# Optimization experiments

Hardware: AMD Instinct MI355X
Metric: run time of the kernel (lower is better)

Reference implementation:

```python
import jax, jax.numpy as jnp
import numpy as np

D_MODEL = 1024
NUM_HEADS = 16
HEAD_DIM = D_MODEL // NUM_HEADS


def setup_inputs() -> dict:
    key = jax.random.key(0)
    ks = jax.random.split(key, 12)
    B, S = 2, 2048
    scale = 1.0 / np.sqrt(D_MODEL)
    inp = {
        "x": jax.random.normal(ks[0], (B, S, D_MODEL), dtype=jnp.float32),
        "docking_scores": jax.random.uniform(ks[1], (B, S), dtype=jnp.float32),
        "q_w": jax.random.normal(ks[2], (D_MODEL, D_MODEL), dtype=jnp.float32) * scale,
        "q_b": jnp.zeros((D_MODEL,), dtype=jnp.float32),
        "k_w": jax.random.normal(ks[3], (D_MODEL, D_MODEL), dtype=jnp.float32) * scale,
        "k_b": jnp.zeros((D_MODEL,), dtype=jnp.float32),
        "v_w": jax.random.normal(ks[4], (D_MODEL, D_MODEL), dtype=jnp.float32) * scale,
        "v_b": jnp.zeros((D_MODEL,), dtype=jnp.float32),
        "o_w": jax.random.normal(ks[5], (D_MODEL, D_MODEL), dtype=jnp.float32) * scale,
        "o_b": jnp.zeros((D_MODEL,), dtype=jnp.float32),
        "alpha": jnp.float32(0.5),
    }
    return inp


def reference(x, docking_scores, q_w, q_b, k_w, k_b, v_w, v_b, o_w, o_b, alpha):
    B, S, _ = x.shape
    # Projections; weights stored as (in, out) so y = x @ W + b
    def proj(w, b):
        y = jnp.einsum('bsd,de->bse', x, w) + b
        return y.reshape(B, S, NUM_HEADS, HEAD_DIM).transpose(0, 2, 1, 3)  # (B,H,S,hd)
    Q = proj(q_w, q_b)
    K = proj(k_w, k_b)
    V = proj(v_w, v_b)
    scores = jnp.einsum('bhqd,bhkd->bhqk', Q, K) / np.sqrt(HEAD_DIM)
    attn = jax.nn.softmax(scores, axis=-1)  # (B,H,S,S)
    # post-softmax docking blend, broadcast over heads and query positions
    ds = docking_scores[:, None, None, :]  # (B,1,1,S)
    attn = (1.0 - alpha) * attn + alpha * ds
    ctx = jnp.einsum('bhqk,bhkd->bhqd', attn, V)
    ctx = ctx.transpose(0, 2, 1, 3).reshape(B, S, D_MODEL)
    return jnp.einsum('bsd,de->bse', ctx, o_w) + o_b
```

## Files before the change

kernel.cpp:

```cpp
#include <hip/hip_runtime.h>
#include <hip/hip_bf16.h>

typedef __attribute__((ext_vector_type(8)))  short bf16x8;
typedef __attribute__((ext_vector_type(4)))  float f32x4;
typedef __attribute__((ext_vector_type(16))) float f32x16;
typedef __attribute__((ext_vector_type(4)))  int   i32x4;
typedef __attribute__((ext_vector_type(4)))  unsigned short u16x4;
typedef __attribute__((ext_vector_type(8)))  unsigned short u16x8;

__device__ __forceinline__ unsigned short f2bf(float f) {
    unsigned int u = __builtin_bit_cast(unsigned int, f);
    u += 0x7FFFu + ((u >> 16) & 1u);
    return (unsigned short)(u >> 16);
}
__device__ __forceinline__ float bf2f(unsigned short h) {
    unsigned int u = ((unsigned int)h) << 16;
    return __builtin_bit_cast(float, u);
}
__device__ __forceinline__ bf16x8 ld16(const unsigned short* p) {
    return *reinterpret_cast<const bf16x8*>(p);
}
__device__ __forceinline__ float fexp2(float x) {
    float r; asm("v_exp_f32 %0, %1" : "=v"(r) : "v"(x)); return r;
}
__device__ __forceinline__ float frcp(float x) {
    float r; asm("v_rcp_f32 %0, %1" : "=v"(r) : "v"(x)); return r;
}
__device__ __forceinline__ void pswap(unsigned int& a, unsigned int& b) {
    asm("v_permlane32_swap_b32 %0, %1" : "+v"(a), "+v"(b));
}

__global__ void prep_kernel(const float* __restrict__ x,
                            const float* __restrict__ q_w, const float* __restrict__ k_w,
                            const float* __restrict__ v_w, const float* __restrict__ o_w,
                            unsigned short* __restrict__ WT, unsigned short* __restrict__ xb) {
    __shared__ float tile[32][33];
    const int tx = threadIdx.x, ty = threadIdx.y;
    if (blockIdx.z < 4) {
        const float* W = (blockIdx.z == 0) ? q_w : (blockIdx.z == 1) ? k_w : (blockIdx.z == 2) ? v_w : o_w;
        unsigned short* dst = WT + (size_t)blockIdx.z * 1024 * 1024;
        int n0 = blockIdx.x * 32, k0 = blockIdx.y * 32;
#pragma unroll
        for (int j = 0; j < 4; ++j)
            tile[ty + j*8][tx] = W[(size_t)(k0 + ty + j*8) * 1024 + n0 + tx];
        __syncthreads();
#pragma unroll
        for (int j = 0; j < 4; ++j)
            dst[(size_t)(n0 + ty + j*8) * 1024 + k0 + tx] = f2bf(tile[tx][ty + j*8]);
    } else {
        const int t = ty * 32 + tx;
        const int bid = blockIdx.y * 32 + blockIdx.x;
#pragma unroll
        for (int c = 0; c < 2; ++c) {
            const int i = bid * 512 + c * 256 + t;
            f32x4 a = reinterpret_cast<const f32x4*>(x)[i*2];
            f32x4 b = reinterpret_cast<const f32x4*>(x)[i*2+1];
            u16x8 o;
            o[0]=f2bf(a[0]); o[1]=f2bf(a[1]); o[2]=f2bf(a[2]); o[3]=f2bf(a[3]);
            o[4]=f2bf(b[0]); o[5]=f2bf(b[1]); o[6]=f2bf(b[2]); o[7]=f2bf(b[3]);
            reinterpret_cast<u16x8*>(xb)[i] = o;
        }
    }
}


__global__ __launch_bounds__(256) void gemm_qkv(
    const unsigned short* __restrict__ A,
    const unsigned short* __restrict__ WT,
    const float* __restrict__ qb, const float* __restrict__ kbias, const float* __restrict__ vbias,
    unsigned short* __restrict__ Qo, unsigned short* __restrict__ KFo, unsigned short* __restrict__ VFo)
{
    __shared__ __align__(16) unsigned short As[2][128*64];
    __shared__ __align__(16) unsigned short Bs[2][128*64];
    const int tid = threadIdx.x, lane = tid & 63, w = tid >> 6;
    const int wm = w >> 1, wn = w & 1;
    const int m0 = blockIdx.y * 128, n0 = blockIdx.x * 128;
    const int K = 1024;
    const int sr = tid >> 3, ssl = tid & 7;
    const int ssw = (ssl ^ (sr & 7)) << 3;
    f32x4 acc[4][4] = {};

    auto stage = [&](int buf, int k0) {
#pragma unroll
        for (int j = 0; j < 4; ++j) {
            const int c = j*256 + tid, r = j*32 + sr;
            __builtin_amdgcn_global_load_lds(
                (const __attribute__((address_space(1))) void*)&A[(size_t)(m0+r)*K + k0 + ssw],
                (__attribute__((address_space(3))) void*)&As[buf][(size_t)c*8], 16, 0, 0);
            __builtin_amdgcn_global_load_lds(
                (const __attribute__((address_space(1))) void*)&WT[(size_t)(n0+r)*K + k0 + ssw],
                (__attribute__((address_space(3))) void*)&Bs[buf][(size_t)c*8], 16, 0, 0);
        }
    };

    stage(0, 0);
#pragma unroll 1
    for (int t = 0; t < 16; ++t) {
        __syncthreads();
        if (t < 15) stage((t + 1) & 1, (t + 1) * 64);
        const unsigned short* pa = &As[t & 1][0];
        const unsigned short* pb = &Bs[t & 1][0];
#pragma unroll
        for (int kc = 0; kc < 2; ++kc) {
            bf16x8 af[4], bfr[4];
            const int slog = kc*4 + (lane >> 4);
#pragma unroll
            for (int t2 = 0; t2 < 4; ++t2) {
                const int row = wm*64 + t2*16 + (lane & 15);
                af[t2]  = ld16(&pa[row*64 + ((slog ^ (row & 7)) << 3)]);
                const int col = wn*64 + t2*16 + (lane & 15);
                bfr[t2] = ld16(&pb[col*64 + ((slog ^ (col & 7)) << 3)]);
            }
#pragma unroll
            for (int mt = 0; mt < 4; ++mt)
#pragma unroll
                for (int nt = 0; nt < 4; ++nt)
                    acc[mt][nt] = __builtin_amdgcn_mfma_f32_16x16x32_bf16(af[mt], bfr[nt], acc[mt][nt], 0, 0, 0);
        }
    }
    const int mat = n0 >> 10;
    if (mat == 2) {
#pragma unroll
        for (int mt = 0; mt < 4; ++mt)
#pragma unroll
        for (int nt = 0; nt < 4; ++nt) {
            const int nl = (n0 & 1023) + wn*64 + nt*16 + (lane & 15);
            const int h = nl >> 6, hd = nl & 63;
            const int mbase = m0 + wm*64 + mt*16 + ((lane >> 4) << 2);
            const int b = mbase >> 11, s = mbase & 2047;
            const float bv = vbias[nl];
            u16x4 pk;
#pragma unroll
            for (int r = 0; r < 4; ++r) pk[r] = f2bf(acc[mt][nt][r] + bv);
            const size_t off = (size_t)((b << 4) | h) * 131072 + (s >> 6) * 4096 + (hd >> 5) * 2048
                             + ((s >> 4) & 3) * 512 + ((s >> 3) & 1) * 256 + (hd & 31) * 8 + (s & 7);
            *reinterpret_cast<u16x4*>(&VFo[off]) = pk;
        }
    } else if (mat == 1) {
#pragma unroll
        for (int mt = 0; mt < 4; ++mt)
#pragma unroll
        for (int nt = 0; nt < 4; ++nt) {
            const int nl = (n0 & 1023) + wn*64 + nt*16 + (lane & 15);
            const int h = nl >> 6, hd = nl & 63;
            const int mbase = m0 + wm*64 + mt*16 + ((lane >> 4) << 2);
            const float bv = kbias[nl];
#pragma unroll
            for (int r = 0; r < 4; ++r) {
                const int mm2 = mbase + r, b = mm2 >> 11, s = mm2 & 2047;
                const size_t off = (size_t)((b << 4) | h) * 131072 + (s >> 5) * 2048 + (hd >> 4) * 512
                                 + ((hd >> 3) & 1) * 256 + (s & 31) * 8 + (hd & 7);
                KFo[off] = f2bf(acc[mt][nt][r] + bv);
            }
        }
    } else {
        const float scale = 0.180336881f;
#pragma unroll
        for (int mt = 0; mt < 4; ++mt)
#pragma unroll
        for (int nt = 0; nt < 4; ++nt) {
            const int nl = (n0 & 1023) + wn*64 + nt*16 + (lane & 15);
            const int h = nl >> 6, hd = nl & 63;
            const int mbase = m0 + wm*64 + mt*16 + ((lane >> 4) << 2);
            const float bv = qb[nl];
#pragma unroll
            for (int r = 0; r < 4; ++r) {
                const int mm2 = mbase + r, b = mm2 >> 11, s = mm2 & 2047;
                Qo[((size_t)((b << 4) | h) * 2048 + s) * 64 + hd] = f2bf((acc[mt][nt][r] + bv) * scale);
            }
        }
    }
}

__global__ __launch_bounds__(256) void gemm_o(
    const unsigned short* __restrict__ A, const unsigned short* __restrict__ WT,
    const float* __restrict__ bias, float* __restrict__ Cout)
{
    __shared__ __align__(16) unsigned short As[2][128*64];
    __shared__ __align__(16) unsigned short Bs[2][128*64];
    const int tid = threadIdx.x, lane = tid & 63, w = tid >> 6;
    const int wm = w >> 1, wn = w & 1;
    const int m0 = blockIdx.y * 128, n0 = blockIdx.x * 128;
    const int K = 1024;
    const int sr = tid >> 3, ssl = tid & 7;
    const int ssw = (ssl ^ (sr & 7)) << 3;
    f32x4 acc[4][4] = {};

    auto stage = [&](int buf, int k0) {
#pragma unroll
        for (int j = 0; j < 4; ++j) {
            const int c = j*256 + tid, r = j*32 + sr;
            __builtin_amdgcn_global_load_lds(
                (const __attribute__((address_space(1))) void*)&A[(size_t)(m0+r)*K + k0 + ssw],
                (__attribute__((address_space(3))) void*)&As[buf][(size_t)c*8], 16, 0, 0);
            __builtin_amdgcn_global_load_lds(
                (const __attribute__((address_space(1))) void*)&WT[(size_t)(n0+r)*K + k0 + ssw],
                (__attribute__((address_space(3))) void*)&Bs[buf][(size_t)c*8], 16, 0, 0);
        }
    };

    stage(0, 0);
#pragma unroll 1
    for (int t = 0; t < 16; ++t) {
        __syncthreads();
        if (t < 15) stage((t + 1) & 1, (t + 1) * 64);
        const unsigned short* pa = &As[t & 1][0];
        const unsigned short* pb = &Bs[t & 1][0];
#pragma unroll
        for (int kc = 0; kc < 2; ++kc) {
            bf16x8 af[4], bfr[4];
            const int slog = kc*4 + (lane >> 4);
#pragma unroll
            for (int t2 = 0; t2 < 4; ++t2) {
                const int row = wm*64 + t2*16 + (lane & 15);
                af[t2]  = ld16(&pa[row*64 + ((slog ^ (row & 7)) << 3)]);
                const int col = wn*64 + t2*16 + (lane & 15);
                bfr[t2] = ld16(&pb[col*64 + ((slog ^ (col & 7)) << 3)]);
            }
#pragma unroll
            for (int mt = 0; mt < 4; ++mt)
#pragma unroll
                for (int nt = 0; nt < 4; ++nt)
                    acc[mt][nt] = __builtin_amdgcn_mfma_f32_16x16x32_bf16(af[mt], bfr[nt], acc[mt][nt], 0, 0, 0);
        }
    }
#pragma unroll
    for (int mt = 0; mt < 4; ++mt)
#pragma unroll
    for (int nt = 0; nt < 4; ++nt) {
        const int n = n0 + wn*64 + nt*16 + (lane & 15);
        const int mbase = m0 + wm*64 + mt*16 + ((lane >> 4) << 2);
        const float bv = bias[n];
#pragma unroll
        for (int r = 0; r < 4; ++r)
            Cout[(size_t)(mbase + r) * 1024 + n] = acc[mt][nt][r] + bv;
    }
}

__global__ void dock_c_kernel(const float* __restrict__ ds, const unsigned short* __restrict__ VF,
                              float* __restrict__ cvec) {
    __shared__ float red[256];
    const int bh = blockIdx.x;
    const int b = bh >> 4;
    const int t = threadIdx.x;
    const int lane = t & 63, t2 = (t >> 6) & 1, k4 = t >> 7;
    const int hi = lane >> 5;
    const unsigned short* VFb = VF + (size_t)bh * 131072;
    const float* dsb = ds + b * 2048;
    float sum = 0.f;
    for (int kvt = k4; kvt < 32; kvt += 2) {
#pragma unroll
        for (int ks = 0; ks < 4; ++ks) {
            bf16x8 v = ld16(VFb + kvt*4096 + t2*2048 + ks*512 + lane*8);
            const int kv0 = kvt*64 + ks*16 + hi*8;
            f32x4 d0 = *reinterpret_cast<const f32x4*>(&dsb[kv0]);
            f32x4 d1 = *reinterpret_cast<const f32x4*>(&dsb[kv0 + 4]);
            sum += d0[0]*bf2f((unsigned short)v[0]) + d0[1]*bf2f((unsigned short)v[1])
                 + d0[2]*bf2f((unsigned short)v[2]) + d0[3]*bf2f((unsigned short)v[3])
                 + d1[0]*bf2f((unsigned short)v[4]) + d1[1]*bf2f((unsigned short)v[5])
                 + d1[2]*bf2f((unsigned short)v[6]) + d1[3]*bf2f((unsigned short)v[7]);
        }
    }
    red[t] = sum;
    __syncthreads();
    if (t < 64) {
        const int ln = t & 31, tt2 = t >> 5;
        const int base = tt2 * 64 + ln;
        cvec[bh * 64 + tt2 * 32 + ln] = red[base] + red[base + 32] + red[base + 128] + red[base + 160];
    }
}

__global__ __launch_bounds__(256, 2) void attn_kernel(
    const unsigned short* __restrict__ Qp,
    const unsigned short* __restrict__ KF,
    const unsigned short* __restrict__ VF,
    const float* __restrict__ cvec,
    const float* __restrict__ alpha_p,
    unsigned short* __restrict__ ctx)
{
    __shared__ __align__(16) unsigned short Ks[2][4096];
    __shared__ __align__(16) unsigned short Vs[2][4096];
    const int tid = threadIdx.x, lane = tid & 63, w = tid >> 6;
    const int hi = lane >> 5, ln = lane & 31;
    const int wg = blockIdx.x;
    const int swz = (wg & 7) * 64 + (wg >> 3);
    const int bh = swz >> 4, qt = swz & 15;
    const int q0 = qt * 128 + w * 32;
    const size_t hb = (size_t)bh * (2048 * 64);
    const float alpha = *alpha_p;

    const unsigned short* KFb = KF + (size_t)bh * 131072;
    const unsigned short* VFb = VF + (size_t)bh * 131072;
    const int fo = lane * 8;

    bf16x8 qf[4];
    {
        const unsigned short* qr = &Qp[hb + (size_t)(q0 + ln) * 64 + hi * 8];
#pragma unroll
        for (int ks = 0; ks < 4; ++ks) qf[ks] = ld16(qr + ks * 16);
    }

    const short one_bf = (short)0x3F80;
    const bf16x8 onesf = {one_bf, one_bf, one_bf, one_bf, one_bf, one_bf, one_bf, one_bf};

    f32x16 oacc0 = {}, oacc1 = {}, lacc = {};

    auto stage = [&](int buf, int it) {
#pragma unroll
        for (int p = 0; p < 2; ++p) {
            __builtin_amdgcn_global_load_lds(
                (const __attribute__((address_space(1))) void*)(KFb + it*4096 + p*2048 + tid*8),
                (__attribute__((address_space(3))) void*)&Ks[buf][p*2048 + tid*8], 16, 0, 0);
            __builtin_amdgcn_global_load_lds(
                (const __attribute__((address_space(1))) void*)(VFb + it*4096 + p*2048 + tid*8),
                (__attribute__((address_space(3))) void*)&Vs[buf][p*2048 + tid*8], 16, 0, 0);
        }
    };

    bf16x8 kf[8];
    auto ldk = [&](const unsigned short* base) {
#pragma unroll
        for (int t2 = 0; t2 < 2; ++t2)
#pragma unroll
        for (int ks = 0; ks < 4; ++ks)
            kf[t2*4+ks] = ld16(base + t2*2048 + ks*512 + fo);
    };

    stage(0, 0);
    __syncthreads();
    stage(1, 1);
    ldk(&Ks[0][0]);
    f32x16 sA0 = {}, sA1 = {}, sB0 = {}, sB1 = {};
#pragma unroll
    for (int ks = 0; ks < 4; ++ks) {
        sA0 = __builtin_amdgcn_mfma_f32_32x32x16_bf16(kf[ks],   qf[ks], sA0, 0, 0, 0);
        sA1 = __builtin_amdgcn_mfma_f32_32x32x16_bf16(kf[4+ks], qf[ks], sA1, 0, 0, 0);
    }

    auto step = [&](f32x16& sc0, f32x16& sc1, f32x16& sn0, f32x16& sn1, int buf, int it) {
        bf16x8 vf[8];
#pragma unroll
        for (int t2 = 0; t2 < 2; ++t2)
#pragma unroll
        for (int ks = 0; ks < 4; ++ks)
            vf[t2*4+ks] = ld16(&Vs[buf][t2*2048 + ks*512 + fo]);
        __syncthreads();
        if (it + 2 < 32) stage(buf, it + 2);
        const bool more = (it + 1 < 32);
        if (more) ldk(&Ks[buf ^ 1][0]);
        __builtin_amdgcn_s_setprio(1);
        if (more) {
            sn0 = {}; sn1 = {};
#pragma unroll
            for (int ks = 0; ks < 4; ++ks) {
                sn0 = __builtin_amdgcn_mfma_f32_32x32x16_bf16(kf[ks],   qf[ks], sn0, 0, 0, 0);
                sn1 = __builtin_amdgcn_mfma_f32_32x32x16_bf16(kf[4+ks], qf[ks], sn1, 0, 0, 0);
            }
        }
        float p0a[16], p1a[16];
#pragma unroll
        for (int r = 0; r < 16; ++r) {
            p0a[r] = fexp2(sc0[r]);
            p1a[r] = fexp2(sc1[r]);
        }
        unsigned int Wp0[4][2], Wp1[4][2];
#pragma unroll
        for (int m4 = 0; m4 < 4; ++m4)
#pragma unroll
        for (int jj = 0; jj < 2; ++jj) {
            asm("v_cvt_pk_bf16_f32 %0, %1, %2" : "=v"(Wp0[m4][jj]) : "v"(p0a[m4*4+jj*2]), "v"(p0a[m4*4+jj*2+1]));
            asm("v_cvt_pk_bf16_f32 %0, %1, %2" : "=v"(Wp1[m4][jj]) : "v"(p1a[m4*4+jj*2]), "v"(p1a[m4*4+jj*2+1]));
        }
#pragma unroll
        for (int ks = 0; ks < 4; ++ks) {
            const int tp = ks & 1;
            unsigned int a0, a1, b0, b1;
            if (ks < 2) { a0 = Wp0[2*tp][0]; a1 = Wp0[2*tp][1]; b0 = Wp0[2*tp+1][0]; b1 = Wp0[2*tp+1][1]; }
            else        { a0 = Wp1[2*tp][0]; a1 = Wp1[2*tp][1]; b0 = Wp1[2*tp+1][0]; b1 = Wp1[2*tp+1][1]; }
            pswap(a0, b0);
            pswap(a1, b1);
            i32x4 pw;
            pw[0] = (int)a0; pw[1] = (int)a1; pw[2] = (int)b0; pw[3] = (int)b1;
            bf16x8 pf = __builtin_bit_cast(bf16x8, pw);
            oacc0 = __builtin_amdgcn_mfma_f32_32x32x16_bf16(pf, vf[ks],   oacc0, 0, 0, 0);
            oacc1 = __builtin_amdgcn_mfma_f32_32x32x16_bf16(pf, vf[4+ks], oacc1, 0, 0, 0);
            lacc  = __builtin_amdgcn_mfma_f32_32x32x16_bf16(pf, onesf,    lacc,  0, 0, 0);
        }
        __builtin_amdgcn_s_setprio(0);
    };

#pragma unroll 1
    for (int ii = 0; ii < 16; ++ii) {
        step(sA0, sA1, sB0, sB1, 0, ii*2);
        step(sB0, sB1, sA0, sA1, 1, ii*2 + 1);
    }

    const int b = bh >> 4, h = bh & 15;
    const float a1f = 1.f - alpha;
    const float cv0 = alpha * cvec[bh*64 + ln];
    const float cv1 = alpha * cvec[bh*64 + 32 + ln];
#pragma unroll
    for (int m4 = 0; m4 < 4; ++m4) {
#pragma unroll
        for (int r3 = 0; r3 < 4; ++r3) {
            const int row = m4*8 + hi*4 + r3;
            const int s = q0 + row;
            const float iv = frcp(lacc[m4*4 + r3]);
            unsigned short* orow = &ctx[((size_t)(b*2048 + s))*1024 + h*64 + ln];
            orow[0]  = f2bf(a1f * oacc0[m4*4+r3] * iv + cv0);
            orow[32] = f2bf(a1f * oacc1[m4*4+r3] * iv + cv1);
        }
    }
}

extern "C" void kernel_launch(void* const* d_in, const int* in_sizes, int n_in,
                              void* d_out, int out_size, void* d_ws, size_t ws_size,
                              hipStream_t stream) {
    const float* x     = (const float*)d_in[0];
    const float* ds    = (const float*)d_in[1];
    const float* q_w   = (const float*)d_in[2];
    const float* q_b   = (const float*)d_in[3];
    const float* k_w   = (const float*)d_in[4];
    const float* k_b   = (const float*)d_in[5];
    const float* v_w   = (const float*)d_in[6];
    const float* v_b   = (const float*)d_in[7];
    const float* o_w   = (const float*)d_in[8];
    const float* o_b   = (const float*)d_in[9];
    const float* alpha = (const float*)d_in[10];

    char* ws = (char*)d_ws;
    const size_t MB = 1024 * 1024;
    unsigned short* xb   = (unsigned short*)(ws);
    unsigned short* wT   = (unsigned short*)(ws + 8  * MB);
    unsigned short* Qb   = (unsigned short*)(ws + 16 * MB);
    unsigned short* KFb  = (unsigned short*)(ws + 24 * MB);
    unsigned short* VFb  = (unsigned short*)(ws + 32 * MB);
    float*          cvec = (float*)         (ws + 40 * MB);
    unsigned short* ctxb = xb;

    dim3 tb(32, 8);
    dim3 tg(32, 32, 5);
    prep_kernel<<<tg, tb, 0, stream>>>(x, q_w, k_w, v_w, o_w, wT, xb);

    dim3 gqkv(24, 32);
    gemm_qkv<<<gqkv, 256, 0, stream>>>(xb, wT, q_b, k_b, v_b, Qb, KFb, VFb);

    dock_c_kernel<<<32, 256, 0, stream>>>(ds, VFb, cvec);

    attn_kernel<<<512, 256, 0, stream>>>(Qb, KFb, VFb, cvec, alpha, ctxb);

    dim3 go(8, 32);
    gemm_o<<<go, 256, 0, stream>>>(ctxb, wT + (size_t)3 * MB, o_b, (float*)d_out);
}
```

Baseline: 126.3 us.

## Double KV tile size per stage to halve barriers in attention loop

The attention kernel now stages two 64-key K/V tiles per LDS buffer (8192 elements each), so each loop iteration processes 128 keys with one barrier and one async global-to-LDS stage instead of two. QK for the second half-tile overlaps softmax/PV of the first half, and QK for the next buffer overlaps the second half's PV. LDS use doubles to 64 KB per block, which may limit the two-blocks-per-CU occupancy target.

```diff
diff --git a/kernel.cpp b/kernel.cpp
--- a/kernel.cpp
+++ b/kernel.cpp
@@ -278,8 +278,8 @@
     const float* __restrict__ alpha_p,
     unsigned short* __restrict__ ctx)
 {
-    __shared__ __align__(16) unsigned short Ks[2][4096];
-    __shared__ __align__(16) unsigned short Vs[2][4096];
+    __shared__ __align__(16) unsigned short Ks[2][8192];
+    __shared__ __align__(16) unsigned short Vs[2][8192];
     const int tid = threadIdx.x, lane = tid & 63, w = tid >> 6;
     const int hi = lane >> 5, ln = lane & 31;
     const int wg = blockIdx.x;
@@ -305,58 +305,42 @@
 
     f32x16 oacc0 = {}, oacc1 = {}, lacc = {};
 
-    auto stage = [&](int buf, int it) {
-#pragma unroll
-        for (int p = 0; p < 2; ++p) {
-            __builtin_amdgcn_global_load_lds(
-                (const __attribute__((address_space(1))) void*)(KFb + it*4096 + p*2048 + tid*8),
+    auto stage2 = [&](int buf, int t2) {
+#pragma unroll
+        for (int p = 0; p < 4; ++p) {
+            __builtin_amdgcn_global_load_lds(
+                (const __attribute__((address_space(1))) void*)(KFb + t2*8192 + p*2048 + tid*8),
                 (__attribute__((address_space(3))) void*)&Ks[buf][p*2048 + tid*8], 16, 0, 0);
             __builtin_amdgcn_global_load_lds(
-                (const __attribute__((address_space(1))) void*)(VFb + it*4096 + p*2048 + tid*8),
+                (const __attribute__((address_space(1))) void*)(VFb + t2*8192 + p*2048 + tid*8),
                 (__attribute__((address_space(3))) void*)&Vs[buf][p*2048 + tid*8], 16, 0, 0);
         }
     };
 
     bf16x8 kf[8];
-    auto ldk = [&](const unsigned short* base) {
+    auto qk = [&](const unsigned short* base, f32x16& s0, f32x16& s1) {
 #pragma unroll
         for (int t2 = 0; t2 < 2; ++t2)
 #pragma unroll
         for (int ks = 0; ks < 4; ++ks)
             kf[t2*4+ks] = ld16(base + t2*2048 + ks*512 + fo);
-    };
-
-    stage(0, 0);
-    __syncthreads();
-    stage(1, 1);
-    ldk(&Ks[0][0]);
-    f32x16 sA0 = {}, sA1 = {}, sB0 = {}, sB1 = {};
-#pragma unroll
-    for (int ks = 0; ks < 4; ++ks) {
-        sA0 = __builtin_amdgcn_mfma_f32_32x32x16_bf16(kf[ks],   qf[ks], sA0, 0, 0, 0);
-        sA1 = __builtin_amdgcn_mfma_f32_32x32x16_bf16(kf[4+ks], qf[ks], sA1, 0, 0, 0);
-    }
-
-    auto step = [&](f32x16& sc0, f32x16& sc1, f32x16& sn0, f32x16& sn1, int buf, int it) {
-        bf16x8 vf[8];
+        s0 = {}; s1 = {};
+#pragma unroll
+        for (int ks = 0; ks < 4; ++ks) {
+            s0 = __builtin_amdgcn_mfma_f32_32x32x16_bf16(kf[ks],   qf[ks], s0, 0, 0, 0);
+            s1 = __builtin_amdgcn_mfma_f32_32x32x16_bf16(kf[4+ks], qf[ks], s1, 0, 0, 0);
+        }
+    };
+
+    auto ldv = [&](bf16x8 (&vf)[8], const unsigned short* base) {
 #pragma unroll
         for (int t2 = 0; t2 < 2; ++t2)
 #pragma unroll
         for (int ks = 0; ks < 4; ++ks)
-            vf[t2*4+ks] = ld16(&Vs[buf][t2*2048 + ks*512 + fo]);
-        __syncthreads();
-        if (it + 2 < 32) stage(buf, it + 2);
-        const bool more = (it + 1 < 32);
-        if (more) ldk(&Ks[buf ^ 1][0]);
-        __builtin_amdgcn_s_setprio(1);
-        if (more) {
-            sn0 = {}; sn1 = {};
-#pragma unroll
-            for (int ks = 0; ks < 4; ++ks) {
-                sn0 = __builtin_amdgcn_mfma_f32_32x32x16_bf16(kf[ks],   qf[ks], sn0, 0, 0, 0);
-                sn1 = __builtin_amdgcn_mfma_f32_32x32x16_bf16(kf[4+ks], qf[ks], sn1, 0, 0, 0);
-            }
-        }
+            vf[t2*4+ks] = ld16(base + t2*2048 + ks*512 + fo);
+    };
+
+    auto smpv = [&](f32x16& sc0, f32x16& sc1, bf16x8 (&vf)[8]) {
         float p0a[16], p1a[16];
 #pragma unroll
         for (int r = 0; r < 16; ++r) {
@@ -386,13 +370,30 @@
             oacc1 = __builtin_amdgcn_mfma_f32_32x32x16_bf16(pf, vf[4+ks], oacc1, 0, 0, 0);
             lacc  = __builtin_amdgcn_mfma_f32_32x32x16_bf16(pf, onesf,    lacc,  0, 0, 0);
         }
-        __builtin_amdgcn_s_setprio(0);
-    };
+    };
+
+    stage2(0, 0);
+    __syncthreads();
+    stage2(1, 1);
+    f32x16 sA0, sA1, sB0, sB1;
+    qk(&Ks[0][0], sA0, sA1);
 
 #pragma unroll 1
     for (int ii = 0; ii < 16; ++ii) {
-        step(sA0, sA1, sB0, sB1, 0, ii*2);
-        step(sB0, sB1, sA0, sA1, 1, ii*2 + 1);
+        const int b = ii & 1;
+        bf16x8 vf0[8], vf1[8];
+        ldv(vf0, &Vs[b][0]);
+        __builtin_amdgcn_s_setprio(1);
+        qk(&Ks[b][4096], sB0, sB1);
+        smpv(sA0, sA1, vf0);
+        __builtin_amdgcn_s_setprio(0);
+        ldv(vf1, &Vs[b][4096]);
+        __syncthreads();
+        if (ii + 2 < 16) stage2(b, ii + 2);
+        __builtin_amdgcn_s_setprio(1);
+        if (ii + 1 < 16) qk(&Ks[b ^ 1][0], sA0, sA1);
+        smpv(sB0, sB1, vf1);
+        __builtin_amdgcn_s_setprio(0);
     }
 
     const int b = bh >> 4, h = bh & 15;
```

Result: no change. 126.6 us (+0.3%).

## Fuse docking dot-product into QKV epilogue and replace ones-MFMA row sum

Applied to the files above, without the earlier changes.

Removes the separate dock_c_kernel by accumulating docking-weighted V sums with atomicAdd in the V-projection epilogue of gemm_qkv, after zeroing cvec with a memset. In attention, the softmax denominator is now computed by scalar adds of the exp values plus a lane swap and shared-memory broadcast, instead of an extra MFMA against a ones vector. This drops one kernel launch and a third of the PV MFMAs per step. In exchange it adds many global atomics (with nondeterministic summation order), a memset, and VALU adds in the inner loop.

```diff
diff --git a/kernel.cpp b/kernel.cpp
--- a/kernel.cpp
+++ b/kernel.cpp
@@ -68,7 +68,9 @@
     const unsigned short* __restrict__ A,
     const unsigned short* __restrict__ WT,
     const float* __restrict__ qb, const float* __restrict__ kbias, const float* __restrict__ vbias,
-    unsigned short* __restrict__ Qo, unsigned short* __restrict__ KFo, unsigned short* __restrict__ VFo)
+    const float* __restrict__ dsv,
+    unsigned short* __restrict__ Qo, unsigned short* __restrict__ KFo, unsigned short* __restrict__ VFo,
+    float* __restrict__ cvec)
 {
     __shared__ __align__(16) unsigned short As[2][128*64];
     __shared__ __align__(16) unsigned short Bs[2][128*64];
@@ -130,11 +132,15 @@
             const int b = mbase >> 11, s = mbase & 2047;
             const float bv = vbias[nl];
             u16x4 pk;
-#pragma unroll
-            for (int r = 0; r < 4; ++r) pk[r] = f2bf(acc[mt][nt][r] + bv);
+            float v0 = acc[mt][nt][0] + bv, v1 = acc[mt][nt][1] + bv;
+            float v2 = acc[mt][nt][2] + bv, v3 = acc[mt][nt][3] + bv;
+            pk[0] = f2bf(v0); pk[1] = f2bf(v1); pk[2] = f2bf(v2); pk[3] = f2bf(v3);
             const size_t off = (size_t)((b << 4) | h) * 131072 + (s >> 6) * 4096 + (hd >> 5) * 2048
                              + ((s >> 4) & 3) * 512 + ((s >> 3) & 1) * 256 + (hd & 31) * 8 + (s & 7);
             *reinterpret_cast<u16x4*>(&VFo[off]) = pk;
+            f32x4 d4 = *reinterpret_cast<const f32x4*>(&dsv[b * 2048 + s]);
+            float part = d4[0]*v0 + d4[1]*v1 + d4[2]*v2 + d4[3]*v3;
+            atomicAdd(&cvec[(size_t)((b << 4) | h) * 64 + hd], part);
         }
     } else if (mat == 1) {
 #pragma unroll
@@ -237,39 +243,6 @@
     }
 }
 
-__global__ void dock_c_kernel(const float* __restrict__ ds, const unsigned short* __restrict__ VF,
-                              float* __restrict__ cvec) {
-    __shared__ float red[256];
-    const int bh = blockIdx.x;
-    const int b = bh >> 4;
-    const int t = threadIdx.x;
-    const int lane = t & 63, t2 = (t >> 6) & 1, k4 = t >> 7;
-    const int hi = lane >> 5;
-    const unsigned short* VFb = VF + (size_t)bh * 131072;
-    const float* dsb = ds + b * 2048;
-    float sum = 0.f;
-    for (int kvt = k4; kvt < 32; kvt += 2) {
-#pragma unroll
-        for (int ks = 0; ks < 4; ++ks) {
-            bf16x8 v = ld16(VFb + kvt*4096 + t2*2048 + ks*512 + lane*8);
-            const int kv0 = kvt*64 + ks*16 + hi*8;
-            f32x4 d0 = *reinterpret_cast<const f32x4*>(&dsb[kv0]);
-            f32x4 d1 = *reinterpret_cast<const f32x4*>(&dsb[kv0 + 4]);
-            sum += d0[0]*bf2f((unsigned short)v[0]) + d0[1]*bf2f((unsigned short)v[1])
-                 + d0[2]*bf2f((unsigned short)v[2]) + d0[3]*bf2f((unsigned short)v[3])
-                 + d1[0]*bf2f((unsigned short)v[4]) + d1[1]*bf2f((unsigned short)v[5])
-                 + d1[2]*bf2f((unsigned short)v[6]) + d1[3]*bf2f((unsigned short)v[7]);
-        }
-    }
-    red[t] = sum;
-    __syncthreads();
-    if (t < 64) {
-        const int ln = t & 31, tt2 = t >> 5;
-        const int base = tt2 * 64 + ln;
-        cvec[bh * 64 + tt2 * 32 + ln] = red[base] + red[base + 32] + red[base + 128] + red[base + 160];
-    }
-}
-
 __global__ __launch_bounds__(256, 2) void attn_kernel(
     const unsigned short* __restrict__ Qp,
     const unsigned short* __restrict__ KF,
@@ -280,6 +253,7 @@
 {
     __shared__ __align__(16) unsigned short Ks[2][4096];
     __shared__ __align__(16) unsigned short Vs[2][4096];
+    __shared__ float sml[4][32];
     const int tid = threadIdx.x, lane = tid & 63, w = tid >> 6;
     const int hi = lane >> 5, ln = lane & 31;
     const int wg = blockIdx.x;
@@ -300,10 +274,8 @@
         for (int ks = 0; ks < 4; ++ks) qf[ks] = ld16(qr + ks * 16);
     }
 
-    const short one_bf = (short)0x3F80;
-    const bf16x8 onesf = {one_bf, one_bf, one_bf, one_bf, one_bf, one_bf, one_bf, one_bf};
-
-    f32x16 oacc0 = {}, oacc1 = {}, lacc = {};
+    f32x16 oacc0 = {}, oacc1 = {};
+    float lsum = 0.f;
 
     auto stage = [&](int buf, int it) {
 #pragma unroll
@@ -362,6 +334,13 @@
         for (int r = 0; r < 16; ++r) {
             p0a[r] = fexp2(sc0[r]);
             p1a[r] = fexp2(sc1[r]);
+        }
+        {
+            float s8[8];
+#pragma unroll
+            for (int r = 0; r < 8; ++r)
+                s8[r] = (p0a[r] + p0a[r+8]) + (p1a[r] + p1a[r+8]);
+            lsum += ((s8[0]+s8[1])+(s8[2]+s8[3])) + ((s8[4]+s8[5])+(s8[6]+s8[7]));
         }
         unsigned int Wp0[4][2], Wp1[4][2];
 #pragma unroll
@@ -384,7 +363,6 @@
             bf16x8 pf = __builtin_bit_cast(bf16x8, pw);
             oacc0 = __builtin_amdgcn_mfma_f32_32x32x16_bf16(pf, vf[ks],   oacc0, 0, 0, 0);
             oacc1 = __builtin_amdgcn_mfma_f32_32x32x16_bf16(pf, vf[4+ks], oacc1, 0, 0, 0);
-            lacc  = __builtin_amdgcn_mfma_f32_32x32x16_bf16(pf, onesf,    lacc,  0, 0, 0);
         }
         __builtin_amdgcn_s_setprio(0);
     };
@@ -395,20 +373,26 @@
         step(sB0, sB1, sA0, sA1, 1, ii*2 + 1);
     }
 
+    {
+        unsigned int ua = __builtin_bit_cast(unsigned int, lsum), ub = ua;
+        pswap(ua, ub);
+        float lw = __builtin_bit_cast(float, ua) + __builtin_bit_cast(float, ub);
+        if (hi == 0) sml[w][ln] = frcp(lw);
+    }
     const int b = bh >> 4, h = bh & 15;
     const float a1f = 1.f - alpha;
     const float cv0 = alpha * cvec[bh*64 + ln];
     const float cv1 = alpha * cvec[bh*64 + 32 + ln];
 #pragma unroll
     for (int m4 = 0; m4 < 4; ++m4) {
+        f32x4 iv4 = *reinterpret_cast<const f32x4*>(&sml[w][m4*8 + hi*4]);
 #pragma unroll
         for (int r3 = 0; r3 < 4; ++r3) {
             const int row = m4*8 + hi*4 + r3;
             const int s = q0 + row;
-            const float iv = frcp(lacc[m4*4 + r3]);
             unsigned short* orow = &ctx[((size_t)(b*2048 + s))*1024 + h*64 + ln];
-            orow[0]  = f2bf(a1f * oacc0[m4*4+r3] * iv + cv0);
-            orow[32] = f2bf(a1f * oacc1[m4*4+r3] * iv + cv1);
+            orow[0]  = f2bf(a1f * oacc0[m4*4+r3] * iv4[r3] + cv0);
+            orow[32] = f2bf(a1f * oacc1[m4*4+r3] * iv4[r3] + cv1);
         }
     }
 }
@@ -442,10 +426,10 @@
     dim3 tg(32, 32, 5);
     prep_kernel<<<tg, tb, 0, stream>>>(x, q_w, k_w, v_w, o_w, wT, xb);
 
+    hipMemsetAsync(cvec, 0, 32 * 64 * sizeof(float), stream);
+
     dim3 gqkv(24, 32);
-    gemm_qkv<<<gqkv, 256, 0, stream>>>(xb, wT, q_b, k_b, v_b, Qb, KFb, VFb);
-
-    dock_c_kernel<<<32, 256, 0, stream>>>(ds, VFb, cvec);
+    gemm_qkv<<<gqkv, 256, 0, stream>>>(xb, wT, q_b, k_b, v_b, ds, Qb, KFb, VFb, cvec);
 
     attn_kernel<<<512, 256, 0, stream>>>(Qb, KFb, VFb, cvec, alpha, ctxb);
 
```

Measured after the change: 165.9 us. 31.4% more time.
